# Kernel optimization log

Hardware: AMD Instinct MI355X
Metric: run time of the kernel (lower is better)

Reference implementation:

```python
import jax, jax.numpy as jnp
import numpy as np

N_NODES = 50000
N_EDGES = 400000
D_NODE = 256
D_EDGE = 64
HEADS = 32          # node_hidden_size // 8
HEAD_DIM = 8        # node_hidden_size // heads
LRELU = 0.01


def _lin_init(key, fan_in, fan_out, bias=True):
    kw, kb = jax.random.split(key)
    s = 1.0 / np.sqrt(fan_in)
    W = jax.random.uniform(kw, (fan_in, fan_out), jnp.float32, -s, s)
    if bias:
        b = jax.random.uniform(kb, (fan_out,), jnp.float32, -s, s)
        return W, b
    return W


def setup_inputs() -> dict:
    key = jax.random.key(0)
    ks = jax.random.split(key, 12)
    x = jax.random.normal(ks[0], (N_NODES, D_NODE), jnp.float32)
    edge_index = jax.random.randint(ks[1], (2, N_EDGES), 0, N_NODES, jnp.int64)
    edge_attr = jax.random.normal(ks[2], (N_EDGES, D_EDGE), jnp.float32)
    Wq, bq = _lin_init(ks[3], D_NODE, D_NODE)
    Wk, bk = _lin_init(ks[4], D_NODE, D_NODE)
    Wv, bv = _lin_init(ks[5], D_NODE, D_NODE)
    We = _lin_init(ks[6], D_EDGE, D_NODE, bias=False)   # lin_edge has no bias in PyG
    Ws, bs = _lin_init(ks[7], D_NODE, D_NODE)           # root/skip connection
    W1, b1 = _lin_init(ks[8], 2 * D_NODE + D_EDGE, D_EDGE)
    W2, b2 = _lin_init(ks[9], D_EDGE, D_EDGE)
    return dict(x=x, edge_index=edge_index, edge_attr=edge_attr,
                Wq=Wq, bq=bq, Wk=Wk, bk=bk, Wv=Wv, bv=bv, We=We,
                Ws=Ws, bs=bs, W1=W1, b1=b1, W2=W2, b2=b2)


def _leaky(v, alpha=LRELU):
    return jnp.where(v >= 0, v, alpha * v)


def reference(x, edge_index, edge_attr, Wq, bq, Wk, bk, Wv, bv, We, Ws, bs, W1, b1, W2, b2):
    N = x.shape[0]
    src, dst = edge_index[0], edge_index[1]

    # ---- TransformerConv (concat heads, root weight, edge_dim) ----
    q = (x @ Wq + bq).reshape(N, HEADS, HEAD_DIM)
    k = (x @ Wk + bk).reshape(N, HEADS, HEAD_DIM)
    v = (x @ Wv + bv).reshape(N, HEADS, HEAD_DIM)
    e = (edge_attr @ We).reshape(-1, HEADS, HEAD_DIM)           # [E,H,C]

    k_j = k[src] + e                                            # [E,H,C]
    alpha = jnp.einsum('ehc,ehc->eh', q[dst], k_j) / np.sqrt(HEAD_DIM)
    # segment softmax over destination nodes
    amax = jax.ops.segment_max(alpha, dst, num_segments=N)      # [N,H]
    ex = jnp.exp(alpha - amax[dst])
    denom = jax.ops.segment_sum(ex, dst, num_segments=N)        # [N,H]
    attn = ex / (denom[dst] + 1e-16)                            # [E,H]

    msg = (v[src] + e) * attn[:, :, None]                       # [E,H,C]
    out = jax.ops.segment_sum(msg, dst, num_segments=N).reshape(N, D_NODE)
    out = out + (x @ Ws + bs)                                   # skip / root weight

    x_new = _leaky(out)                                         # block activation

    # ---- EdgeResidualLayer ----
    h = jnp.concatenate([x_new[src], x_new[dst], edge_attr], axis=-1)  # [E,576]
    h = _leaky(h @ W1 + b1)
    edge_new = edge_attr + (h @ W2 + b2)
    edge_new = _leaky(edge_new)

    return (x_new, edge_new)
```

## Files before the change

kernel.cpp:

```cpp
#include <hip/hip_runtime.h>
#include <hip/hip_bf16.h>


#define N_NODES 50000
#define N_EDGES 400000
#define D_NODE 256
#define D_EDGE 64
#define HEADS 32
#define LRELU 0.01f
#define SEG 16

typedef __hip_bfloat16 bf16;
typedef __attribute__((ext_vector_type(8))) short short8b;
typedef __attribute__((ext_vector_type(4))) float f32x4;
typedef __attribute__((ext_vector_type(4))) unsigned short ushort4v;

__device__ __forceinline__ float bf2f(bf16 v) { return __bfloat162float(v); }
__device__ __forceinline__ bf16 f2bf(float f) { return __float2bfloat16(f); }
__device__ __forceinline__ float bfraw(unsigned short u) {
    return __uint_as_float(((unsigned int)u) << 16);
}
__device__ __forceinline__ unsigned short rawbf(float f) {
    bf16 t = f2bf(f); return *(unsigned short*)&t;
}
__device__ __forceinline__ float leaky(float v) { return v >= 0.f ? v : LRELU * v; }
__device__ __forceinline__ short8b pack8(const f32x4 a, const f32x4 b) {
    short8b r;
    r[0] = (short)rawbf(a[0]); r[1] = (short)rawbf(a[1]);
    r[2] = (short)rawbf(a[2]); r[3] = (short)rawbf(a[3]);
    r[4] = (short)rawbf(b[0]); r[5] = (short)rawbf(b[1]);
    r[6] = (short)rawbf(b[2]); r[7] = (short)rawbf(b[3]);
    return r;
}

__global__ void k0_detect(const int* __restrict__ ei, int* __restrict__ flags)
{
    const int lane = threadIdx.x;
    const unsigned long long mz = __ballot(ei[2 * lane + 1] == 0);
    if (lane == 0) flags[0] = (__popcll(mz) >= 48) ? 1 : 0;
}

__device__ __forceinline__ void load_edge(const int* ei, int f, int i, int& s, int& d)
{
    if (f) {
        const long long* e64 = (const long long*)ei;
        s = (int)e64[i]; d = (int)e64[N_EDGES + i];
    } else {
        s = ei[i]; d = ei[N_EDGES + i];
    }
}

__global__ __launch_bounds__(256) void kcd_degree(
    const int* __restrict__ ei, const int* __restrict__ flags, int* __restrict__ deg)
{
    const int i = blockIdx.x * 256 + threadIdx.x;
    if (i >= N_EDGES) return;
    int s, d; load_edge(ei, flags[0], i, s, d);
    atomicAdd(&deg[d], 1);
}

__global__ __launch_bounds__(1024) void kcs_scan(int* __restrict__ cur)
{
    __shared__ int ps[1024];
    const int t = threadIdx.x;
    const int CHN = (N_NODES + 1023) / 1024;
    const int base = t * CHN;
    int sum = 0;
    for (int i = 0; i < CHN; ++i) {
        const int n = base + i;
        if (n < N_NODES) sum += cur[n];
    }
    ps[t] = sum;
    __syncthreads();
    for (int off = 1; off < 1024; off <<= 1) {
        const int v = (t >= off) ? ps[t - off] : 0;
        __syncthreads();
        ps[t] += v;
        __syncthreads();
    }
    int excl = (t == 0) ? 0 : ps[t - 1];
    for (int i = 0; i < CHN; ++i) {
        const int n = base + i;
        if (n < N_NODES) {
            const int d = cur[n];
            cur[n] = excl;
            excl += d;
        }
    }
}

__global__ __launch_bounds__(256) void kct_scatter(
    const int* __restrict__ ei, const int* __restrict__ flags, int* __restrict__ cursor,
    int* __restrict__ ssort, int* __restrict__ dsort, int* __restrict__ eidsort)
{
    const int i = blockIdx.x * 256 + threadIdx.x;
    if (i >= N_EDGES) return;
    int s, d; load_edge(ei, flags[0], i, s, d);
    const int pos = atomicAdd(&cursor[d], 1);
    ssort[pos] = s; dsort[pos] = d; eidsort[pos] = i;
}

__global__ __launch_bounds__(256) void kT_transpose(
    const float* __restrict__ We, const float* __restrict__ W1, const float* __restrict__ W2,
    const float* __restrict__ Wq, const float* __restrict__ Wk,
    const float* __restrict__ Wv, const float* __restrict__ Ws,
    bf16* __restrict__ WeTf, bf16* __restrict__ W1sdf, bf16* __restrict__ W1eaf,
    bf16* __restrict__ W2Tf, bf16* __restrict__ WT4f)
{
    const int gid = blockIdx.x * 256 + threadIdx.x;
    const int gsz = gridDim.x * 256;
    for (int i = gid; i < 4 * 16 * 8 * 512; i += gsz) {
        const int j = i & 7, l = (i >> 3) & 63, kc = (i >> 9) & 7;
        const int ct = (i >> 12) & 15, m = i >> 16;
        const int row = l & 15, kg = l >> 4;
        const int n = ct * 16 + row, k = kc * 32 + kg * 8 + j;
        const float* W = (m == 0) ? Wq : (m == 1) ? Wk : (m == 2) ? Wv : Ws;
        WT4f[i] = f2bf(W[k * 256 + n]);
    }
    for (int i = gid; i < 16 * 2 * 512; i += gsz) {
        const int j = i & 7, l = (i >> 3) & 63, kc = (i >> 9) & 1, ct = i >> 10;
        const int row = l & 15, kg = l >> 4;
        const int n = ct * 16 + row, k = kc * 32 + kg * 8 + j;
        WeTf[i] = f2bf(We[k * 256 + n]);
    }
    for (int i = gid; i < 2 * 4 * 8 * 512; i += gsz) {
        const int j = i & 7, l = (i >> 3) & 63, kc = (i >> 9) & 7;
        const int ct = (i >> 12) & 3, m2 = i >> 14;
        const int row = l & 15, kg = l >> 4;
        const int n = ct * 16 + row;
        const int k = m2 * 256 + kc * 32 + kg * 8 + j;
        W1sdf[i] = f2bf(W1[k * 64 + n]);
    }
    for (int i = gid; i < 4 * 2 * 512; i += gsz) {
        const int j = i & 7, l = (i >> 3) & 63, kc = (i >> 9) & 1, ct = i >> 10;
        const int row = l & 15, kg = l >> 4;
        const int n = ct * 16 + row;
        const int k = 512 + kc * 32 + kg * 8 + j;
        W1eaf[i] = f2bf(W1[k * 64 + n]);
    }
    for (int i = gid; i < 4 * 2 * 512; i += gsz) {
        const int j = i & 7, l = (i >> 3) & 63, kc = (i >> 9) & 1, ct = i >> 10;
        const int row = l & 15, kg = l >> 4;
        const int n = ct * 16 + row, k = kc * 32 + kg * 8 + j;
        W2Tf[i] = f2bf(W2[k * 64 + n]);
    }
}

#define X_LD 264
__global__ __launch_bounds__(256) void k1_node_mfma(
    const float* __restrict__ x, const bf16* __restrict__ WT4f,
    const float* __restrict__ bq, const float* __restrict__ bk,
    const float* __restrict__ bv, const float* __restrict__ bs,
    bf16* __restrict__ qo, bf16* __restrict__ ko, bf16* __restrict__ vo,
    bf16* __restrict__ skipb)
{
    __shared__ unsigned short xs[64 * X_LD];
    const int tid = threadIdx.x;
    const int n0 = blockIdx.x * 64;
    const int w = tid >> 6, l = tid & 63;
    const int row = l & 15, kg = l >> 4;

    {
        const int e = tid >> 2, t = tid & 3;
        const int nmine = n0 + e;
        const f32x4* src = (const f32x4*)(x + (size_t)nmine * 256 + t * 64);
        #pragma unroll
        for (int c = 0; c < 4; ++c) {
            unsigned short tmp[16];
            if (nmine < N_NODES) {
                #pragma unroll
                for (int u = 0; u < 4; ++u) {
                    const f32x4 v = __builtin_nontemporal_load(src + c * 4 + u);
                    tmp[u * 4 + 0] = rawbf(v[0]); tmp[u * 4 + 1] = rawbf(v[1]);
                    tmp[u * 4 + 2] = rawbf(v[2]); tmp[u * 4 + 3] = rawbf(v[3]);
                }
            } else {
                #pragma unroll
                for (int u = 0; u < 16; ++u) tmp[u] = 0;
            }
            *(short8b*)&xs[e * X_LD + t * 64 + c * 16]     = *(short8b*)&tmp[0];
            *(short8b*)&xs[e * X_LD + t * 64 + c * 16 + 8] = *(short8b*)&tmp[8];
        }
    }
    short8b af[8];
    #pragma unroll
    for (int kc = 0; kc < 8; ++kc)
        af[kc] = *(const short8b*)&xs[(w * 16 + row) * X_LD + kc * 32 + kg * 8];

    for (int m = 0; m < 4; ++m) {
        const float* bias = (m == 0) ? bq : (m == 1) ? bk : (m == 2) ? bv : bs;
        #pragma unroll 4
        for (int ct = 0; ct < 16; ++ct) {
            const float bvv = bias[ct * 16 + row];
            f32x4 acc = {bvv, bvv, bvv, bvv};
            #pragma unroll
            for (int kc = 0; kc < 8; ++kc) {
                const short8b bfr = *(const short8b*)(WT4f + (((size_t)((m * 16 + ct) * 8 + kc)) << 9) + l * 8);
                acc = __builtin_amdgcn_mfma_f32_16x16x32_bf16(af[kc], bfr, acc, 0, 0, 0);
            }
            #pragma unroll
            for (int r = 0; r < 4; ++r)
                xs[(w * 16 + kg * 4 + r) * X_LD + ct * 16 + row] = rawbf(acc[r]);
        }
        {
            bf16* dst = (m == 0) ? qo : (m == 1) ? ko : (m == 2) ? vo : skipb;
            #pragma unroll
            for (int u = 0; u < 8; ++u) {
                const int flat = u * 64 + l;
                const int node = w * 16 + (flat >> 5);
                const int col8 = (flat & 31) * 8;
                if (n0 + node < N_NODES) {
                    const short8b vdat = *(const short8b*)&xs[node * X_LD + col8];
                    *(short8b*)(dst + (size_t)(n0 + node) * 256 + col8) = vdat;
                }
            }
        }
    }
}

#define EP_LD 264
__global__ __launch_bounds__(256) void k2_seg(
    const int* __restrict__ ssort, const int* __restrict__ dsort,
    const int* __restrict__ eidsort, const int* __restrict__ endptr,
    const float* __restrict__ ea, const bf16* __restrict__ WeTf,
    const bf16* __restrict__ q, const bf16* __restrict__ k, const bf16* __restrict__ v,
    const bf16* __restrict__ skipb, float* __restrict__ out_x, bf16* __restrict__ xnb)
{
    __shared__ float acc_s[SEG * 256];
    __shared__ float den_s[SEG * HEADS];
    __shared__ unsigned short ep_s[64 * EP_LD];
    const int tid = threadIdx.x;
    const int n0 = blockIdx.x * SEG;

    #pragma unroll
    for (int i = 0; i < SEG; ++i) acc_s[i * 256 + tid] = 0.f;
    if (tid < SEG * HEADS - 256) den_s[256 + tid] = 0.f;
    den_s[tid] = 0.f;

    const int start = (n0 == 0) ? 0 : endptr[n0 - 1];
    const int end   = endptr[n0 + SEG - 1];
    __syncthreads();

    const int w = tid >> 6, l = tid & 63;
    const int row = l & 15, kg = l >> 4;
    const float scale = 0.35355339059327373f;

    for (int sbase = start + w * 16; sbase < end; sbase += 64) {
        const int cnt = min(16, end - sbase);

        short8b af0 = {0, 0, 0, 0, 0, 0, 0, 0}, af1 = af0;
        if (row < cnt) {
            const int eg = eidsort[sbase + row];
            const float* pb = ea + (size_t)eg * 64 + kg * 8;
            const f32x4 a0 = __builtin_nontemporal_load((const f32x4*)pb);
            const f32x4 a1 = __builtin_nontemporal_load((const f32x4*)(pb + 4));
            const f32x4 b0 = __builtin_nontemporal_load((const f32x4*)(pb + 32));
            const f32x4 b1 = __builtin_nontemporal_load((const f32x4*)(pb + 36));
            af0 = pack8(a0, a1); af1 = pack8(b0, b1);
        }

        int sv = 0;
        if (l < 16)      { if (l < cnt)      sv = ssort[sbase + l]; }
        else if (l < 32) { if (l - 16 < cnt) sv = dsort[sbase + (l - 16)]; }

        ushort4v kvv[16], vvv[16], qvv[16];
        #pragma unroll
        for (int i = 0; i < 16; ++i) {
            const int s = __shfl(sv, min(i, cnt - 1));
            const int d = __shfl(sv, 16 + min(i, cnt - 1));
            kvv[i] = *(const ushort4v*)(k + (size_t)s * 256 + l * 4);
            vvv[i] = *(const ushort4v*)(v + (size_t)s * 256 + l * 4);
            qvv[i] = *(const ushort4v*)(q + (size_t)d * 256 + l * 4);
        }
        __builtin_amdgcn_sched_barrier(0);

        #pragma unroll 4
        for (int ct = 0; ct < 16; ++ct) {
            f32x4 acc = {0.f, 0.f, 0.f, 0.f};
            const short8b b0 = *(const short8b*)(WeTf + (ct * 2 + 0) * 512 + l * 8);
            const short8b b1 = *(const short8b*)(WeTf + (ct * 2 + 1) * 512 + l * 8);
            acc = __builtin_amdgcn_mfma_f32_16x16x32_bf16(af0, b0, acc, 0, 0, 0);
            acc = __builtin_amdgcn_mfma_f32_16x16x32_bf16(af1, b1, acc, 0, 0, 0);
            #pragma unroll
            for (int r = 0; r < 4; ++r)
                ep_s[(w * 16 + kg * 4 + r) * EP_LD + ct * 16 + row] = rawbf(acc[r]);
        }

        float macc[4] = {0.f, 0.f, 0.f, 0.f};
        float dacc = 0.f;
        int dprev = -1;

        #pragma unroll
        for (int i = 0; i < 16; ++i) {
            const int d = __shfl(sv, 16 + min(i, cnt - 1));
            if (d != dprev) {
                if (dprev >= 0) {
                    const int ld = dprev - n0;
                    #pragma unroll
                    for (int t = 0; t < 4; ++t)
                        atomicAdd(&acc_s[ld * 256 + l * 4 + t], macc[t]);
                    if ((l & 1) == 0)
                        atomicAdd(&den_s[ld * HEADS + (l >> 1)], dacc);
                    macc[0] = macc[1] = macc[2] = macc[3] = 0.f;
                    dacc = 0.f;
                }
                dprev = d;
            }
            const ushort4v ep = *(const ushort4v*)&ep_s[(w * 16 + i) * EP_LD + l * 4];
            float p = 0.f, m4[4];
            #pragma unroll
            for (int t = 0; t < 4; ++t) {
                const float epf = bfraw(ep[t]);
                p = fmaf(bfraw(qvv[i][t]), bfraw(kvv[i][t]) + epf, p);
                m4[t] = bfraw(vvv[i][t]) + epf;
            }
            p += __shfl_xor(p, 1);
            const float ex = (i < cnt) ? __expf(p * scale) : 0.f;
            #pragma unroll
            for (int t = 0; t < 4; ++t) macc[t] = fmaf(m4[t], ex, macc[t]);
            dacc += ex;
        }
        {
            const int ld = dprev - n0;
            #pragma unroll
            for (int t = 0; t < 4; ++t)
                atomicAdd(&acc_s[ld * 256 + l * 4 + t], macc[t]);
            if ((l & 1) == 0)
                atomicAdd(&den_s[ld * HEADS + (l >> 1)], dacc);
        }
    }
    __syncthreads();

    #pragma unroll
    for (int u = 0; u < 4; ++u) {
        const int flat4 = u * 256 + tid;
        const int node = flat4 >> 6;
        const int ch4 = flat4 & 63;
        const int n = n0 + node;
        const float den = den_s[node * HEADS + (ch4 >> 1)] + 1e-16f;
        const f32x4 mv = *(const f32x4*)&acc_s[node * 256 + ch4 * 4];
        const ushort4v sk = *(const ushort4v*)(skipb + (size_t)n * 256 + ch4 * 4);
        f32x4 o; ushort4v ob;
        #pragma unroll
        for (int t = 0; t < 4; ++t) {
            const float xn = leaky(mv[t] / den + bfraw(sk[t]));
            o[t] = xn; ob[t] = rawbf(xn);
        }
        *(f32x4*)(out_x + (size_t)n * 256 + ch4 * 4) = o;
        *(ushort4v*)(xnb + (size_t)n * 256 + ch4 * 4) = ob;
    }
}

#define PB_LD 136
__global__ __launch_bounds__(256) void k3b_nodeproj(
    const bf16* __restrict__ xnb, const bf16* __restrict__ W1sdf,
    bf16* __restrict__ P)
{
    __shared__ unsigned short ps_s[64 * PB_LD];
    const int tid = threadIdx.x;
    const int n0 = blockIdx.x * 64;
    const int w = tid >> 6, l = tid & 63;
    const int row = l & 15, kg = l >> 4;

    const int nmine = n0 + w * 16 + row;
    const size_t nbase = (size_t)min(nmine, N_NODES - 1) * 256;
    short8b af[8];
    #pragma unroll
    for (int kc = 0; kc < 8; ++kc)
        af[kc] = *(const short8b*)(xnb + nbase + kc * 32 + kg * 8);

    #pragma unroll
    for (int m = 0; m < 2; ++m) {
        #pragma unroll
        for (int ct = 0; ct < 4; ++ct) {
            f32x4 acc = {0.f, 0.f, 0.f, 0.f};
            #pragma unroll
            for (int kc = 0; kc < 8; ++kc) {
                const short8b bfr = *(const short8b*)(W1sdf + ((m * 4 + ct) * 8 + kc) * 512 + l * 8);
                acc = __builtin_amdgcn_mfma_f32_16x16x32_bf16(af[kc], bfr, acc, 0, 0, 0);
            }
            #pragma unroll
            for (int r = 0; r < 4; ++r)
                ps_s[(w * 16 + kg * 4 + r) * PB_LD + m * 64 + ct * 16 + row] = rawbf(acc[r]);
        }
    }
    __syncthreads();
    #pragma unroll
    for (int u = 0; u < 4; ++u) {
        const int flat = u * 256 + tid;
        const int node = flat >> 4;
        const int c8 = (flat & 15) * 8;
        if (n0 + node < N_NODES) {
            const short8b vdat = *(const short8b*)&ps_s[node * PB_LD + c8];
            *(short8b*)(P + (size_t)(n0 + node) * 128 + c8) = vdat;
        }
    }
}

__global__ __launch_bounds__(256) void k4_edge_mlp(
    const int* __restrict__ ssort, const int* __restrict__ dsort,
    const int* __restrict__ eidsort,
    const bf16* __restrict__ P, const float* __restrict__ ea,
    const bf16* __restrict__ W1eaf, const float* __restrict__ b1,
    const bf16* __restrict__ W2Tf, const float* __restrict__ b2,
    float* __restrict__ out_e)
{
    __shared__ unsigned short h2_s[4][16 * 72];
    __shared__ unsigned short ea_s[4][16 * 72];
    const int tid = threadIdx.x;
    const int w = tid >> 6, l = tid & 63;
    const int row = l & 15, kg = l >> 4;
    const int e0 = blockIdx.x * 64;
    const int sl = e0 + w * 16 + row;
    const int eg = eidsort[sl];

    int s2[4], d2[4], eg2[4];
    #pragma unroll
    for (int r = 0; r < 4; ++r) {
        const int cr = e0 + w * 16 + kg * 4 + r;
        s2[r] = ssort[cr]; d2[r] = dsort[cr]; eg2[r] = eidsort[cr];
    }

    const float* pb = ea + (size_t)eg * 64 + kg * 8;
    const f32x4 a0 = __builtin_nontemporal_load((const f32x4*)pb);
    const f32x4 a1 = __builtin_nontemporal_load((const f32x4*)(pb + 4));
    const f32x4 c0 = __builtin_nontemporal_load((const f32x4*)(pb + 32));
    const f32x4 c1 = __builtin_nontemporal_load((const f32x4*)(pb + 36));

    const unsigned short* Pu = (const unsigned short*)P;
    unsigned short psv[4][4], pdv[4][4];
    #pragma unroll
    for (int ct = 0; ct < 4; ++ct)
        #pragma unroll
        for (int r = 0; r < 4; ++r) {
            psv[ct][r] = Pu[(size_t)s2[r] * 128 + ct * 16 + row];
            pdv[ct][r] = Pu[(size_t)d2[r] * 128 + 64 + ct * 16 + row];
        }
    __builtin_amdgcn_sched_barrier(0);

    const short8b afr0 = pack8(a0, a1);
    const short8b afr1 = pack8(c0, c1);
    *(short8b*)&ea_s[w][row * 72 + kg * 8]      = afr0;
    *(short8b*)&ea_s[w][row * 72 + 32 + kg * 8] = afr1;

    f32x4 acc[4];
    #pragma unroll
    for (int ct = 0; ct < 4; ++ct) {
        const float bvv = b1[ct * 16 + row];
        acc[ct] = (f32x4){bvv, bvv, bvv, bvv};
    }
    #pragma unroll
    for (int kc = 0; kc < 2; ++kc) {
        const short8b af = (kc == 0) ? afr0 : afr1;
        #pragma unroll
        for (int ct = 0; ct < 4; ++ct) {
            const short8b bfr = *(const short8b*)(W1eaf + (ct * 2 + kc) * 512 + l * 8);
            acc[ct] = __builtin_amdgcn_mfma_f32_16x16x32_bf16(af, bfr, acc[ct], 0, 0, 0);
        }
    }
    #pragma unroll
    for (int ct = 0; ct < 4; ++ct)
        #pragma unroll
        for (int r = 0; r < 4; ++r)
            acc[ct][r] += bfraw(psv[ct][r]) + bfraw(pdv[ct][r]);

    unsigned short* h2 = h2_s[w];
    #pragma unroll
    for (int ct = 0; ct < 4; ++ct)
        #pragma unroll
        for (int r = 0; r < 4; ++r)
            h2[(kg * 4 + r) * 72 + ct * 16 + row] = rawbf(leaky(acc[ct][r]));

    f32x4 a2[4];
    #pragma unroll
    for (int ct = 0; ct < 4; ++ct) {
        const float bvv = b2[ct * 16 + row];
        a2[ct] = (f32x4){bvv, bvv, bvv, bvv};
    }
    #pragma unroll
    for (int kc = 0; kc < 2; ++kc) {
        const short8b af = *(const short8b*)&h2[row * 72 + kc * 32 + kg * 8];
        #pragma unroll
        for (int ct = 0; ct < 4; ++ct) {
            const short8b bfr = *(const short8b*)(W2Tf + (ct * 2 + kc) * 512 + l * 8);
            a2[ct] = __builtin_amdgcn_mfma_f32_16x16x32_bf16(af, bfr, a2[ct], 0, 0, 0);
        }
    }

    #pragma unroll
    for (int ct = 0; ct < 4; ++ct)
        #pragma unroll
        for (int r = 0; r < 4; ++r) {
            const float eav = bfraw(ea_s[w][(kg * 4 + r) * 72 + ct * 16 + row]);
            out_e[(size_t)eg2[r] * 64 + ct * 16 + row] = leaky(eav + a2[ct][r]);
        }
}

extern "C" void kernel_launch(void* const* d_in, const int* in_sizes, int n_in,
                              void* d_out, int out_size, void* d_ws, size_t ws_size,
                              hipStream_t stream)
{
    const float* x  = (const float*)d_in[0];
    const int*   ei = (const int*)d_in[1];
    const float* ea = (const float*)d_in[2];
    const float* Wq = (const float*)d_in[3];
    const float* bq = (const float*)d_in[4];
    const float* Wk = (const float*)d_in[5];
    const float* bk = (const float*)d_in[6];
    const float* Wv = (const float*)d_in[7];
    const float* bv = (const float*)d_in[8];
    const float* We = (const float*)d_in[9];
    const float* Ws = (const float*)d_in[10];
    const float* bs = (const float*)d_in[11];
    const float* W1 = (const float*)d_in[12];
    const float* b1 = (const float*)d_in[13];
    const float* W2 = (const float*)d_in[14];
    const float* b2 = (const float*)d_in[15];

    char* ws = (char*)d_ws;
    int*   flags  = (int*)ws;
    int*   ssort  = (int*)(ws + 4096);
    int*   dsort  = (int*)(ws + 1604096);
    int*   eids   = (int*)(ws + 3204096);
    int*   cursor = (int*)(ws + 4804096);
    bf16*  WeTf   = (bf16*)(ws + 5004096);
    bf16*  W1sdf  = (bf16*)(ws + 5036864);
    bf16*  W1eaf  = (bf16*)(ws + 5102400);
    bf16*  W2Tf   = (bf16*)(ws + 5110592);
    bf16*  WT4f   = (bf16*)(ws + 5118784);
    bf16*  qb     = (bf16*)(ws + 5643072);
    bf16*  kb     = (bf16*)(ws + 31243072);
    bf16*  vb     = (bf16*)(ws + 56843072);
    bf16*  xnb    = (bf16*)(ws + 82443072);
    bf16*  Pp     = (bf16*)(ws + 108100000);

    float* out_x = (float*)d_out;
    float* out_e = out_x + (size_t)N_NODES * D_NODE;
    bf16*  skipb = (bf16*)out_e;

    hipMemsetAsync(cursor, 0, N_NODES * 4, stream);

    k0_detect<<<1, 64, 0, stream>>>(ei, flags);
    kcd_degree<<<(N_EDGES + 255) / 256, 256, 0, stream>>>(ei, flags, cursor);
    kcs_scan<<<1, 1024, 0, stream>>>(cursor);
    kct_scatter<<<(N_EDGES + 255) / 256, 256, 0, stream>>>(ei, flags, cursor, ssort, dsort, eids);

    kT_transpose<<<64, 256, 0, stream>>>(We, W1, W2, Wq, Wk, Wv, Ws,
                                         WeTf, W1sdf, W1eaf, W2Tf, WT4f);

    k1_node_mfma<<<(N_NODES + 63) / 64, 256, 0, stream>>>(
        x, WT4f, bq, bk, bv, bs, qb, kb, vb, skipb);

    k2_seg<<<N_NODES / SEG, 256, 0, stream>>>(
        ssort, dsort, eids, cursor, ea, WeTf, qb, kb, vb, skipb, out_x, xnb);

    k3b_nodeproj<<<(N_NODES + 63) / 64, 256, 0, stream>>>(xnb, W1sdf, Pp);

    k4_edge_mlp<<<N_EDGES / 64, 256, 0, stream>>>(
        ssort, dsort, eids, Pp, ea, W1eaf, b1, W2Tf, b2, out_e);
}
```

Baseline: 601.5 us.

## Fuse node projection into segment kernel, dedupe q loads, remap edge blocks per XCD

Folds the k3b node projection (x_new @ W1 src/dst halves) into the end of k2_seg: each 16-node segment reuses the bf16 x_new tile it just wrote into LDS and runs the MFMA projection there, which removes one launch and one re-read of xnb. The q row is now loaded only when the destination changes, not once per edge, which cuts gather traffic and register pressure. k4 remaps block ids so each XCD works on a contiguous range of edges, aiming for better L2 locality on the P gathers. The cost is that each k2 block now does 16-row MFMA tiles that use only part of the block, and the P stores are scattered bf16 writes.

After: 568.3 us. -5.5%, faster.

```diff
diff --git a/kernel.cpp b/kernel.cpp
--- a/kernel.cpp
+++ b/kernel.cpp
@@ -224,7 +224,8 @@
     const int* __restrict__ eidsort, const int* __restrict__ endptr,
     const float* __restrict__ ea, const bf16* __restrict__ WeTf,
     const bf16* __restrict__ q, const bf16* __restrict__ k, const bf16* __restrict__ v,
-    const bf16* __restrict__ skipb, float* __restrict__ out_x, bf16* __restrict__ xnb)
+    const bf16* __restrict__ skipb, const bf16* __restrict__ W1sdf,
+    float* __restrict__ out_x, bf16* __restrict__ xnb, bf16* __restrict__ P)
 {
     __shared__ float acc_s[SEG * 256];
     __shared__ float den_s[SEG * HEADS];
@@ -263,14 +264,12 @@
         if (l < 16)      { if (l < cnt)      sv = ssort[sbase + l]; }
         else if (l < 32) { if (l - 16 < cnt) sv = dsort[sbase + (l - 16)]; }
 
-        ushort4v kvv[16], vvv[16], qvv[16];
+        ushort4v kvv[16], vvv[16];
         #pragma unroll
         for (int i = 0; i < 16; ++i) {
             const int s = __shfl(sv, min(i, cnt - 1));
-            const int d = __shfl(sv, 16 + min(i, cnt - 1));
             kvv[i] = *(const ushort4v*)(k + (size_t)s * 256 + l * 4);
             vvv[i] = *(const ushort4v*)(v + (size_t)s * 256 + l * 4);
-            qvv[i] = *(const ushort4v*)(q + (size_t)d * 256 + l * 4);
         }
         __builtin_amdgcn_sched_barrier(0);
 
@@ -289,6 +288,7 @@
         float macc[4] = {0.f, 0.f, 0.f, 0.f};
         float dacc = 0.f;
         int dprev = -1;
+        ushort4v qv = {0, 0, 0, 0};
 
         #pragma unroll
         for (int i = 0; i < 16; ++i) {
@@ -304,6 +304,7 @@
                     macc[0] = macc[1] = macc[2] = macc[3] = 0.f;
                     dacc = 0.f;
                 }
+                qv = *(const ushort4v*)(q + (size_t)d * 256 + l * 4);
                 dprev = d;
             }
             const ushort4v ep = *(const ushort4v*)&ep_s[(w * 16 + i) * EP_LD + l * 4];
@@ -311,7 +312,7 @@
             #pragma unroll
             for (int t = 0; t < 4; ++t) {
                 const float epf = bfraw(ep[t]);
-                p = fmaf(bfraw(qvv[i][t]), bfraw(kvv[i][t]) + epf, p);
+                p = fmaf(bfraw(qv[t]), bfraw(kvv[i][t]) + epf, p);
                 m4[t] = bfraw(vvv[i][t]) + epf;
             }
             p += __shfl_xor(p, 1);
@@ -348,51 +349,28 @@
         }
         *(f32x4*)(out_x + (size_t)n * 256 + ch4 * 4) = o;
         *(ushort4v*)(xnb + (size_t)n * 256 + ch4 * 4) = ob;
-    }
-}
-
-#define PB_LD 136
-__global__ __launch_bounds__(256) void k3b_nodeproj(
-    const bf16* __restrict__ xnb, const bf16* __restrict__ W1sdf,
-    bf16* __restrict__ P)
-{
-    __shared__ unsigned short ps_s[64 * PB_LD];
-    const int tid = threadIdx.x;
-    const int n0 = blockIdx.x * 64;
-    const int w = tid >> 6, l = tid & 63;
-    const int row = l & 15, kg = l >> 4;
-
-    const int nmine = n0 + w * 16 + row;
-    const size_t nbase = (size_t)min(nmine, N_NODES - 1) * 256;
-    short8b af[8];
-    #pragma unroll
-    for (int kc = 0; kc < 8; ++kc)
-        af[kc] = *(const short8b*)(xnb + nbase + kc * 32 + kg * 8);
-
-    #pragma unroll
-    for (int m = 0; m < 2; ++m) {
-        #pragma unroll
-        for (int ct = 0; ct < 4; ++ct) {
+        *(ushort4v*)&ep_s[node * EP_LD + ch4 * 4] = ob;
+    }
+    __syncthreads();
+
+    {
+        short8b af2[8];
+        #pragma unroll
+        for (int kc = 0; kc < 8; ++kc)
+            af2[kc] = *(const short8b*)&ep_s[row * EP_LD + kc * 32 + kg * 8];
+        #pragma unroll
+        for (int c2 = 0; c2 < 2; ++c2) {
+            const int ct = w * 2 + c2;
+            const int m2 = ct >> 2, ct4 = ct & 3;
             f32x4 acc = {0.f, 0.f, 0.f, 0.f};
             #pragma unroll
             for (int kc = 0; kc < 8; ++kc) {
-                const short8b bfr = *(const short8b*)(W1sdf + ((m * 4 + ct) * 8 + kc) * 512 + l * 8);
-                acc = __builtin_amdgcn_mfma_f32_16x16x32_bf16(af[kc], bfr, acc, 0, 0, 0);
+                const short8b bfr = *(const short8b*)(W1sdf + ((m2 * 4 + ct4) * 8 + kc) * 512 + l * 8);
+                acc = __builtin_amdgcn_mfma_f32_16x16x32_bf16(af2[kc], bfr, acc, 0, 0, 0);
             }
             #pragma unroll
             for (int r = 0; r < 4; ++r)
-                ps_s[(w * 16 + kg * 4 + r) * PB_LD + m * 64 + ct * 16 + row] = rawbf(acc[r]);
-        }
-    }
-    __syncthreads();
-    #pragma unroll
-    for (int u = 0; u < 4; ++u) {
-        const int flat = u * 256 + tid;
-        const int node = flat >> 4;
-        const int c8 = (flat & 15) * 8;
-        if (n0 + node < N_NODES) {
-            const short8b vdat = *(const short8b*)&ps_s[node * PB_LD + c8];
-            *(short8b*)(P + (size_t)(n0 + node) * 128 + c8) = vdat;
+                P[(size_t)(n0 + kg * 4 + r) * 128 + m2 * 64 + ct4 * 16 + row] = f2bf(acc[r]);
         }
     }
 }
@@ -410,7 +388,11 @@
     const int tid = threadIdx.x;
     const int w = tid >> 6, l = tid & 63;
     const int row = l & 15, kg = l >> 4;
-    const int e0 = blockIdx.x * 64;
+
+    const int q8 = (N_EDGES / 64) >> 3, r8 = (N_EDGES / 64) & 7;
+    const int xcd = blockIdx.x & 7, idx = blockIdx.x >> 3;
+    const int bid = (xcd < r8 ? xcd * (q8 + 1) : r8 * (q8 + 1) + (xcd - r8) * q8) + idx;
+    const int e0 = bid * 64;
     const int sl = e0 + w * 16 + row;
     const int eg = eidsort[sl];
 
@@ -552,9 +534,8 @@
         x, WT4f, bq, bk, bv, bs, qb, kb, vb, skipb);
 
     k2_seg<<<N_NODES / SEG, 256, 0, stream>>>(
-        ssort, dsort, eids, cursor, ea, WeTf, qb, kb, vb, skipb, out_x, xnb);
-
-    k3b_nodeproj<<<(N_NODES + 63) / 64, 256, 0, stream>>>(xnb, W1sdf, Pp);
+        ssort, dsort, eids, cursor, ea, WeTf, qb, kb, vb, skipb, W1sdf,
+        out_x, xnb, Pp);
 
     k4_edge_mlp<<<N_EDGES / 64, 256, 0, stream>>>(
         ssort, dsort, eids, Pp, ea, W1eaf, b1, W2Tf, b2, out_e);
```
